# Performance work log

Hardware: AMD Instinct MI355X
Metric: run time of the kernel (lower is better)

Reference implementation:

```python
import jax, jax.numpy as jnp
import numpy as np

D_MODEL = 256
N_HEADS = 4
WINDOW = 8
DECAY = 0.9
STEP_SIZE = 0.5


def _linear(x, w, b):
    # torch nn.Linear: y = x @ w.T + b, w: [out, in]
    return jnp.einsum('...i,oi->...o', x, w) + b


def _layernorm(x, scale, bias, eps=1e-5):
    mu = jnp.mean(x, axis=-1, keepdims=True)
    var = jnp.var(x, axis=-1, keepdims=True)
    return (x - mu) * jax.lax.rsqrt(var + eps) * scale + bias


def _ema(x, decay):
    # ema[t] = decay*ema[t-1] + (1-decay)*x[t], ema[-1]=0
    # (exactly the causal conv with weights (1-d)*d^i from the torch code)
    def step(c, xt):
        c = decay * c + (1.0 - decay) * xt
        return c, c
    _, ys = jax.lax.scan(step, jnp.zeros_like(x[:, 0]), jnp.swapaxes(x, 0, 1))
    return jnp.swapaxes(ys, 0, 1)


def setup_inputs() -> dict:
    key = jax.random.key(0)
    ks = iter(jax.random.split(key, 40))
    B, T, D = 8, 1024, D_MODEL
    s = 0.02
    inp = {
        'parallel_repr': jax.random.normal(next(ks), (B, T, D), jnp.float32),
        'sequential_state': jax.random.normal(next(ks), (B, D), jnp.float32),
        'trajectory_summary': jax.random.normal(next(ks), (B, D), jnp.float32),
        # MultiheadAttention params
        'in_proj_w': jax.random.normal(next(ks), (3 * D, D), jnp.float32) * s,
        'in_proj_b': jnp.zeros((3 * D,), jnp.float32),
        'out_proj_w': jax.random.normal(next(ks), (D, D), jnp.float32) * s,
        'out_proj_b': jnp.zeros((D,), jnp.float32),
        # depthwise causal conv (local history)
        'conv_w': jax.random.normal(next(ks), (D, 1, WINDOW), jnp.float32) * s,
        'conv_b': jnp.zeros((D,), jnp.float32),
        # parallel_to_sequential / sequential_to_parallel
        'p2s_w': jax.random.normal(next(ks), (D, D), jnp.float32) * s,
        'p2s_b': jnp.zeros((D,), jnp.float32),
        's2p_w': jax.random.normal(next(ks), (D, D), jnp.float32) * s,
        's2p_b': jnp.zeros((D,), jnp.float32),
        # transition MLP: 3D -> 2D -> D
        'trans_w1': jax.random.normal(next(ks), (2 * D, 3 * D), jnp.float32) * s,
        'trans_b1': jnp.zeros((2 * D,), jnp.float32),
        'trans_w2': jax.random.normal(next(ks), (D, 2 * D), jnp.float32) * s,
        'trans_b2': jnp.zeros((D,), jnp.float32),
        # FFN: D -> 4D -> D
        'ffn_w1': jax.random.normal(next(ks), (4 * D, D), jnp.float32) * s,
        'ffn_b1': jnp.zeros((4 * D,), jnp.float32),
        'ffn_w2': jax.random.normal(next(ks), (D, 4 * D), jnp.float32) * s,
        'ffn_b2': jnp.zeros((D,), jnp.float32),
        # LayerNorms
        'ln1_s': jnp.ones((D,), jnp.float32), 'ln1_b': jnp.zeros((D,), jnp.float32),
        'ln2_s': jnp.ones((D,), jnp.float32), 'ln2_b': jnp.zeros((D,), jnp.float32),
        'ln3_s': jnp.ones((D,), jnp.float32), 'ln3_b': jnp.zeros((D,), jnp.float32),
        'ln4_s': jnp.ones((D,), jnp.float32), 'ln4_b': jnp.zeros((D,), jnp.float32),
    }
    return inp


def _forward(parallel_repr, sequential_state,
             in_proj_w, in_proj_b, out_proj_w, out_proj_b,
             conv_w, conv_b, p2s_w, p2s_b, s2p_w, s2p_b,
             trans_w1, trans_b1, trans_w2, trans_b2,
             ffn_w1, ffn_b1, ffn_w2, ffn_b2,
             ln1_s, ln1_b, ln2_s, ln2_b, ln3_s, ln3_b, ln4_s, ln4_b):
    B, T, D = parallel_repr.shape
    H, hd = N_HEADS, D // N_HEADS

    # --- causal self-attention (nn.MultiheadAttention, batch_first) ---
    qkv = _linear(parallel_repr, in_proj_w, in_proj_b)
    q, k, v = jnp.split(qkv, 3, axis=-1)
    q = q.reshape(B, T, H, hd)
    k = k.reshape(B, T, H, hd)
    v = v.reshape(B, T, H, hd)
    scores = jnp.einsum('bqhd,bkhd->bhqk', q, k) / jnp.sqrt(jnp.asarray(hd, q.dtype))
    causal = jnp.triu(jnp.ones((T, T), bool), 1)
    scores = jnp.where(causal, jnp.finfo(scores.dtype).min, scores)
    attn = jax.nn.softmax(scores, axis=-1)
    attn_out = jnp.einsum('bhqk,bkhd->bqhd', attn, v).reshape(B, T, D)
    attn_out = _linear(attn_out, out_proj_w, out_proj_b)
    x = _layernorm(parallel_repr + attn_out, ln1_s, ln1_b)

    # --- depthwise causal conv (local history) ---
    xt = jnp.swapaxes(x, 1, 2)  # [B, D, T]
    xt_pad = jnp.pad(xt, ((0, 0), (0, 0), (WINDOW - 1, 0)))
    local = jax.lax.conv_general_dilated(
        xt_pad, conv_w, window_strides=(1,), padding='VALID',
        dimension_numbers=('NCH', 'OIH', 'NCH'), feature_group_count=D)
    local_history = jnp.swapaxes(local + conv_b[None, :, None], 1, 2)  # [B, T, D]

    # --- global EMA summary ---
    global_summary = _ema(x, DECAY)

    # --- transition deltas + cumsum state integration ---
    parallel_guidance = _linear(x, p2s_w, p2s_b)
    combined = jnp.concatenate([x + 0.3 * parallel_guidance, local_history, global_summary], axis=-1)
    h = jax.nn.gelu(_linear(combined, trans_w1, trans_b1), approximate=False)
    deltas = _linear(h, trans_w2, trans_b2)
    states = sequential_state[:, None, :] + jnp.cumsum(deltas, axis=1) * STEP_SIZE
    states = _layernorm(states, ln3_s, ln3_b)

    # --- FFN with sequential guidance ---
    seq_guidance = _linear(states, s2p_w, s2p_b)
    f = jax.nn.gelu(_linear(x + 0.3 * seq_guidance, ffn_w1, ffn_b1), approximate=False)
    ffn_out = _linear(f, ffn_w2, ffn_b2)
    x = _layernorm(x + ffn_out, ln2_s, ln2_b)

    final_sequential_state = _layernorm(states[:, -1, :], ln4_s, ln4_b)
    final_trajectory_summary = global_summary[:, -1, :]
    return x, final_sequential_state, final_trajectory_summary


def reference(parallel_repr, sequential_state, trajectory_summary,
              in_proj_w, in_proj_b, out_proj_w, out_proj_b,
              conv_w, conv_b, p2s_w, p2s_b, s2p_w, s2p_b,
              trans_w1, trans_b1, trans_w2, trans_b2,
              ffn_w1, ffn_b1, ffn_w2, ffn_b2,
              ln1_s, ln1_b, ln2_s, ln2_b, ln3_s, ln3_b, ln4_s, ln4_b):
    # trajectory_summary is accepted by the torch forward but never used.
    return _forward(parallel_repr, sequential_state,
                    in_proj_w, in_proj_b, out_proj_w, out_proj_b,
                    conv_w, conv_b, p2s_w, p2s_b, s2p_w, s2p_b,
                    trans_w1, trans_b1, trans_w2, trans_b2,
                    ffn_w1, ffn_b1, ffn_w2, ffn_b2,
                    ln1_s, ln1_b, ln2_s, ln2_b, ln3_s, ln3_b, ln4_s, ln4_b)
```

## Files before the change

### kernel.cpp

```cpp
#include <hip/hip_runtime.h>
#include <math.h>

typedef unsigned short u16;
typedef __attribute__((ext_vector_type(8))) short bf16x8;
typedef __attribute__((ext_vector_type(4))) float f32x4;

#define D_MODEL 256
#define T_SZ 1024
constexpr size_t S_ELT = (size_t)8192 * 256;
constexpr size_t MB = 1024 * 1024;

constexpr size_t OFF_QK = 0;
constexpr size_t OFF_VT = 8 * MB;
constexpr size_t OFF_ATTN = 12 * MB;
constexpr size_t OFF_X = 16 * MB;
constexpr size_t OFF_XBF = 24 * MB;
constexpr size_t OFF_COMB = 28 * MB;
constexpr size_t OFF_XP = 36 * MB;
constexpr size_t OFF_H = 40 * MB;
constexpr size_t OFF_FB = 48 * MB;
constexpr size_t OFF_STATES = 56 * MB;
constexpr size_t OFF_FFNIN = 60 * MB;
constexpr size_t OFF_F = 64 * MB;
constexpr size_t OFF_PRBF = 80 * MB;
constexpr size_t OFF_WB = 84 * MB;
constexpr size_t OFF_SCR = 88 * MB;

constexpr int WB_INPROJ = 0;
constexpr int WB_OUTPROJ = 196608;
constexpr int WB_P2S = 262144;
constexpr int WB_S2P = 327680;
constexpr int WB_T1 = 393216;
constexpr int WB_T2 = 786432;
constexpr int WB_F1 = 917504;
constexpr int WB_F2 = 1179648;
constexpr int WB_TOTAL = 1441792;
constexpr int PR_TOTAL = 2097152;

__device__ __forceinline__ u16 f2bf(float f) {
  unsigned int u = __float_as_uint(f);
  u += 0x7fff + ((u >> 16) & 1);
  return (u16)(u >> 16);
}
__device__ __forceinline__ float bf2f(u16 s) {
  return __uint_as_float(((unsigned int)s) << 16);
}

__device__ __forceinline__ void glds16(const u16* g, u16* l) {
  __builtin_amdgcn_global_load_lds(
      (const __attribute__((address_space(1))) void*)g,
      (__attribute__((address_space(3))) void*)l, 16, 0, 0);
}

__device__ __forceinline__ float block_reduce_sum(float v, float* tmp) {
#pragma unroll
  for (int o = 32; o > 0; o >>= 1) v += __shfl_down(v, o);
  const int lane = threadIdx.x & 63, wid = threadIdx.x >> 6;
  if (lane == 0) tmp[wid] = v;
  __syncthreads();
  v = tmp[0] + tmp[1] + tmp[2] + tmp[3];
  __syncthreads();
  return v;
}

__global__ __launch_bounds__(256)
void wconv_kernel(const float* w0, const float* w1, const float* w2,
                  const float* w3, const float* w4, const float* w5,
                  const float* w6, const float* w7, const float* pr,
                  u16* __restrict__ wb, u16* __restrict__ prb) {
  const int idx4 = (blockIdx.x * 256 + threadIdx.x) * 4;
  if (idx4 < WB_TOTAL) {
    const int offs[9] = {WB_INPROJ, WB_OUTPROJ, WB_P2S,  WB_S2P, WB_T1,
                         WB_T2,     WB_F1,      WB_F2,   WB_TOTAL};
    const float* srcs[8] = {w0, w1, w2, w3, w4, w5, w6, w7};
    int seg = 0;
    while (idx4 >= offs[seg + 1]) ++seg;
    float4 v = *(const float4*)(srcs[seg] + (idx4 - offs[seg]));
    unsigned int lo = (unsigned int)f2bf(v.x) | ((unsigned int)f2bf(v.y) << 16);
    unsigned int hi = (unsigned int)f2bf(v.z) | ((unsigned int)f2bf(v.w) << 16);
    *(uint2*)(wb + idx4) = make_uint2(lo, hi);
  } else {
    const int i4 = idx4 - WB_TOTAL;
    if (i4 < PR_TOTAL) {
      float4 v = *(const float4*)(pr + i4);
      unsigned int lo = (unsigned int)f2bf(v.x) | ((unsigned int)f2bf(v.y) << 16);
      unsigned int hi = (unsigned int)f2bf(v.z) | ((unsigned int)f2bf(v.w) << 16);
      *(uint2*)(prb + i4) = make_uint2(lo, hi);
    }
  }
}

enum { EPI_NONE = 0, EPI_GELU = 1, EPI_ADDSCALE = 2 };

template <int EPI, int BM, int BN, bool OUTBF, bool VSPLIT>
__global__ __launch_bounds__(256, 4)
void mgemm(const u16* __restrict__ A1, int lda1, const u16* __restrict__ A2,
           int lda2, int ksplit, const u16* __restrict__ W1, int ldw1,
           const u16* __restrict__ W2, int ldw2, int woff2, int K,
           const float* __restrict__ bias, void* __restrict__ Cv, int ldc,
           const float* __restrict__ addsrc, u16* __restrict__ vt) {
  __shared__ u16 As[BM * 64];
  __shared__ u16 Bs[BN * 64];
  const int tid = threadIdx.x;
  const int w = tid >> 6, lane = tid & 63;
  const int ln = lane & 15, quad = lane >> 4;
  const int m0 = blockIdx.x * BM;
  const int n0 = blockIdx.y * BN;
  constexpr int MT = BM / 64;
  constexpr int NT = BN / 16;
  const int wm = w * (MT * 16);
  constexpr int APW = BM / 64;
  constexpr int BPW = BN / 64;

  f32x4 acc[MT][NT] = {};

  const int grow = lane >> 2;
  const int gk8 = (lane & 3) * 8;

  for (int k0 = 0; k0 < K; k0 += 64) {
#pragma unroll
    for (int s = 0; s < 2; ++s) {
      const int kb = k0 + s * 32;
      const bool r1 = kb < ksplit;
      const u16* Ab = r1 ? A1 : A2;
      const int alda = r1 ? lda1 : lda2;
      const int ak = r1 ? kb : kb - ksplit;
#pragma unroll
      for (int p = 0; p < APW; ++p) {
        const int g = w * APW + p;
        glds16(Ab + (size_t)(m0 + g * 16 + grow) * alda + ak + gk8,
               As + s * BM * 32 + g * 512);
      }
      const u16* Wb = r1 ? W1 : W2;
      const int wlda = r1 ? ldw1 : ldw2;
      const int wk = r1 ? kb : kb - woff2;
#pragma unroll
      for (int p = 0; p < BPW; ++p) {
        const int g = w * BPW + p;
        glds16(Wb + (size_t)(n0 + g * 16 + grow) * wlda + wk + gk8,
               Bs + s * BN * 32 + g * 512);
      }
    }
    __syncthreads();
#pragma unroll
    for (int s = 0; s < 2; ++s) {
      const u16* abase = As + s * BM * 32 + (wm >> 4) * 512 + ln * 32 + quad * 8;
      const u16* bbase = Bs + s * BN * 32 + ln * 32 + quad * 8;
      bf16x8 af[MT], bv[NT];
#pragma unroll
      for (int i = 0; i < MT; ++i) af[i] = *(const bf16x8*)(abase + i * 512);
#pragma unroll
      for (int j = 0; j < NT; ++j) bv[j] = *(const bf16x8*)(bbase + j * 512);
#pragma unroll
      for (int i = 0; i < MT; ++i)
#pragma unroll
        for (int j = 0; j < NT; ++j)
          acc[i][j] = __builtin_amdgcn_mfma_f32_16x16x32_bf16(af[i], bv[j],
                                                              acc[i][j], 0, 0, 0);
    }
    __syncthreads();
  }

#pragma unroll
  for (int i = 0; i < MT; ++i)
#pragma unroll
    for (int j = 0; j < NT; ++j) {
      const int col = n0 + j * 16 + ln;
      const float bsv = bias[col];
      const int row0 = m0 + wm + i * 16 + quad * 4;
      float vals[4];
#pragma unroll
      for (int r = 0; r < 4; ++r) {
        float v = acc[i][j][r] + bsv;
        if (EPI == EPI_GELU) v = 0.5f * v * (1.0f + erff(v * 0.70710678f));
        if (EPI == EPI_ADDSCALE)
          v = addsrc[(size_t)(row0 + r) * 256 + col] + 0.3f * v;
        vals[r] = v;
      }
      if (VSPLIT && col >= 512) {
        ushort4 pk;
        pk.x = f2bf(vals[0]); pk.y = f2bf(vals[1]);
        pk.z = f2bf(vals[2]); pk.w = f2bf(vals[3]);
        *(ushort4*)(vt + (size_t)((row0 >> 10) * 256 + (col - 512)) * T_SZ +
                    (row0 & 1023)) = pk;
      } else if (OUTBF) {
#pragma unroll
        for (int r = 0; r < 4; ++r)
          ((u16*)Cv)[(size_t)(row0 + r) * ldc + col] = f2bf(vals[r]);
      } else {
#pragma unroll
        for (int r = 0; r < 4; ++r)
          ((float*)Cv)[(size_t)(row0 + r) * ldc + col] = vals[r];
      }
    }
}

__global__ __launch_bounds__(256)
void attn_flash(const u16* __restrict__ qk, const u16* __restrict__ vt,
                u16* __restrict__ outp) {
  __shared__ u16 Ps[4][16][72];
  const int tid = threadIdx.x;
  const int w = tid >> 6, lane = tid & 63;
  const int ln = lane & 15, quad = lane >> 4, kq8 = quad * 8;
  const int wu = blockIdx.x * 4 + w;
  const int bh = wu >> 6, s = wu & 63;
  const int qt = (s & 1) ? (63 - (s >> 1)) : (s >> 1);
  const int q0 = qt * 16;
  const int b = bh >> 2, h = bh & 3;
  const u16* base = qk + (size_t)b * T_SZ * 512;
  const u16* vbase = vt + (size_t)bh * 64 * T_SZ;

  bf16x8 qf[2];
#pragma unroll
  for (int ks = 0; ks < 2; ++ks)
    qf[ks] = *(const bf16x8*)(base + (size_t)(q0 + ln) * 512 + h * 64 +
                              ks * 32 + kq8);
  const short ob = (short)0x3F80;
  const bf16x8 ones = {ob, ob, ob, ob, ob, ob, ob, ob};

  f32x4 O[4] = {};
  f32x4 l_acc = {};
  const int ntiles = (qt >> 2) + 1;
  for (int jt = 0; jt < ntiles; ++jt) {
    const int c0 = jt * 64;
    f32x4 sv[4] = {};
#pragma unroll
    for (int ks = 0; ks < 2; ++ks)
#pragma unroll
      for (int j = 0; j < 4; ++j) {
        bf16x8 kf = *(const bf16x8*)(base + (size_t)(c0 + j * 16 + ln) * 512 +
                                     256 + h * 64 + ks * 32 + kq8);
        sv[j] = __builtin_amdgcn_mfma_f32_16x16x32_bf16(qf[ks], kf, sv[j], 0, 0, 0);
      }
    const bool need_mask = (c0 + 63 > q0);
#pragma unroll
    for (int j = 0; j < 4; ++j)
#pragma unroll
      for (int r = 0; r < 4; ++r) {
        float p = __expf(sv[j][r] * 0.125f);
        if (need_mask && (c0 + j * 16 + ln > q0 + quad * 4 + r)) p = 0.f;
        Ps[w][quad * 4 + r][j * 16 + ln] = f2bf(p);
      }
#pragma unroll
    for (int ks = 0; ks < 2; ++ks) {
      bf16x8 pf = *(const bf16x8*)&Ps[w][ln][ks * 32 + kq8];
      l_acc = __builtin_amdgcn_mfma_f32_16x16x32_bf16(pf, ones, l_acc, 0, 0, 0);
#pragma unroll
      for (int j = 0; j < 4; ++j) {
        bf16x8 vf = *(const bf16x8*)(vbase + (size_t)(j * 16 + ln) * T_SZ +
                                     c0 + ks * 32 + kq8);
        O[j] = __builtin_amdgcn_mfma_f32_16x16x32_bf16(pf, vf, O[j], 0, 0, 0);
      }
    }
  }
  u16* op = outp + (size_t)b * T_SZ * 256;
#pragma unroll
  for (int r = 0; r < 4; ++r) {
    const float inv = 1.f / l_acc[r];
#pragma unroll
    for (int j = 0; j < 4; ++j)
      op[(size_t)(q0 + quad * 4 + r) * 256 + h * 64 + j * 16 + ln] =
          f2bf(O[j][r] * inv);
  }
}

__device__ __forceinline__ float ln_finish(float v, float s1, float s2,
                                           float g, float bb) {
  float mean = s1 * (1.f / 256.f);
  float var = s2 * (1.f / 256.f) - mean * mean;
  return (v - mean) * rsqrtf(var + 1e-5f) * g + bb;
}

__global__ __launch_bounds__(256)
void ln_add_kernel(const float* __restrict__ a, const float* __restrict__ addsrc,
                   const float* __restrict__ g, const float* __restrict__ bb,
                   float* __restrict__ outp, u16* __restrict__ obf) {
  __shared__ float tmp[4];
  const size_t row = blockIdx.x;
  const int d = threadIdx.x;
  float v = a[row * 256 + d] + addsrc[row * 256 + d];
  float s1 = block_reduce_sum(v, tmp);
  float s2 = block_reduce_sum(v * v, tmp);
  float y = ln_finish(v, s1, s2, g[d], bb[d]);
  outp[row * 256 + d] = y;
  if (obf) obf[row * 256 + d] = f2bf(y);
}

__global__ __launch_bounds__(256)
void ln34_kernel(const float* __restrict__ deltas, const float* __restrict__ scr,
                 const float* __restrict__ seq, const float* __restrict__ g3,
                 const float* __restrict__ b3, const float* __restrict__ g4,
                 const float* __restrict__ b4, u16* __restrict__ st,
                 float* __restrict__ fss) {
  __shared__ float tmp[4];
  const int row = blockIdx.x;
  const int b = row >> 10, t = row & 1023;
  const int d = threadIdx.x;
  float v = seq[b * 256 + d] +
            0.5f * (deltas[(size_t)row * 256 + d] +
                    scr[(size_t)(b * 32 + (t >> 5)) * 256 + d]);
  float s1 = block_reduce_sum(v, tmp);
  float s2 = block_reduce_sum(v * v, tmp);
  float y = ln_finish(v, s1, s2, g3[d], b3[d]);
  st[(size_t)row * 256 + d] = f2bf(y);
  if (t == 1023) {
    float t1s = block_reduce_sum(y, tmp);
    float t2s = block_reduce_sum(y * y, tmp);
    fss[b * 256 + d] = ln_finish(y, t1s, t2s, g4[d], b4[d]);
  }
}

__global__ __launch_bounds__(256)
void emaconv_kernel(const float* __restrict__ x, const float* __restrict__ cw,
                    const float* __restrict__ cb, u16* __restrict__ comb,
                    float* __restrict__ scr) {
  const int bc = blockIdx.x;
  const int b = bc >> 5, ch = bc & 31;
  const int d = threadIdx.x;
  const int t0 = ch * 32;
  float wreg[8];
#pragma unroll
  for (int j = 0; j < 8; ++j) wreg[j] = cw[d * 8 + j];
  const float bias = cb[d];
  float xw[8];
#pragma unroll
  for (int j = 0; j < 7; ++j) {
    const int ts = t0 - 7 + j;
    xw[j] = (ts >= 0) ? x[(size_t)(b * T_SZ + ts) * 256 + d] : 0.f;
  }
  float c = 0.f;
#pragma unroll
  for (int tl = 0; tl < 32; ++tl) {
    const size_t row = (size_t)(b * T_SZ + t0 + tl);
    xw[7] = x[row * 256 + d];
    float conv = bias;
#pragma unroll
    for (int j = 0; j < 8; ++j) conv = fmaf(xw[j], wreg[j], conv);
    c = 0.9f * c + 0.1f * xw[7];
    comb[row * 512 + d] = f2bf(conv);
    comb[row * 512 + 256 + d] = f2bf(c);
#pragma unroll
    for (int j = 0; j < 7; ++j) xw[j] = xw[j + 1];
  }
  scr[(size_t)bc * 256 + d] = c;
}

__global__ __launch_bounds__(256)
void ema_b_kernel(float* __restrict__ scr) {
  const int b = blockIdx.x, d = threadIdx.x;
  const float q32 = 0.03433683820292512f;
  float carry = 0.f;
  for (int ch = 0; ch < 32; ++ch) {
    const size_t idx = (size_t)(b * 32 + ch) * 256 + d;
    float e = scr[idx];
    scr[idx] = carry;
    carry = e + q32 * carry;
  }
}

__global__ __launch_bounds__(256)
void ema_c_kernel(u16* __restrict__ comb, const float* __restrict__ scr,
                  float* __restrict__ fts) {
  const int row = blockIdx.x;
  const int b = row >> 10, t = row & 1023;
  const int d = threadIdx.x;
  const int ch = t >> 5, tl = t & 31;
  float carry = scr[(size_t)(b * 32 + ch) * 256 + d];
  float l = bf2f(comb[(size_t)row * 512 + 256 + d]);
  float y = fmaf(__powf(0.9f, (float)(tl + 1)), carry, l);
  comb[(size_t)row * 512 + 256 + d] = f2bf(y);
  if (t == 1023) fts[b * 256 + d] = y;
}

__global__ __launch_bounds__(256)
void cs_a_kernel(float* __restrict__ deltas, float* __restrict__ scr) {
  const int bc = blockIdx.x;
  const int b = bc >> 5, ch = bc & 31;
  const int d = threadIdx.x;
  const int t0 = ch * 32;
  float c = 0.f;
  for (int tl = 0; tl < 32; ++tl) {
    const size_t idx = (size_t)(b * T_SZ + t0 + tl) * 256 + d;
    c += deltas[idx];
    deltas[idx] = c;
  }
  scr[(size_t)bc * 256 + d] = c;
}

__global__ __launch_bounds__(256)
void cs_b_kernel(float* __restrict__ scr) {
  const int b = blockIdx.x, d = threadIdx.x;
  float carry = 0.f;
  for (int ch = 0; ch < 32; ++ch) {
    const size_t idx = (size_t)(b * 32 + ch) * 256 + d;
    float e = scr[idx];
    scr[idx] = carry;
    carry += e;
  }
}

extern "C" void kernel_launch(void* const* d_in, const int* in_sizes, int n_in,
                              void* d_out, int out_size, void* d_ws,
                              size_t ws_size, hipStream_t stream) {
  (void)in_sizes; (void)n_in; (void)out_size; (void)ws_size;
  const float* parallel_repr = (const float*)d_in[0];
  const float* sequential_state = (const float*)d_in[1];
  const float* in_proj_b = (const float*)d_in[4];
  const float* out_proj_b = (const float*)d_in[6];
  const float* conv_w = (const float*)d_in[7];
  const float* conv_b = (const float*)d_in[8];
  const float* p2s_b = (const float*)d_in[10];
  const float* s2p_b = (const float*)d_in[12];
  const float* trans_b1 = (const float*)d_in[14];
  const float* trans_b2 = (const float*)d_in[16];
  const float* ffn_b1 = (const float*)d_in[18];
  const float* ffn_b2 = (const float*)d_in[20];
  const float* ln1_s = (const float*)d_in[21];
  const float* ln1_b = (const float*)d_in[22];
  const float* ln2_s = (const float*)d_in[23];
  const float* ln2_b = (const float*)d_in[24];
  const float* ln3_s = (const float*)d_in[25];
  const float* ln3_b = (const float*)d_in[26];
  const float* ln4_s = (const float*)d_in[27];
  const float* ln4_b = (const float*)d_in[28];

  char* ws = (char*)d_ws;
  u16* qk_bf = (u16*)(ws + OFF_QK);
  u16* vt = (u16*)(ws + OFF_VT);
  u16* attn_bf = (u16*)(ws + OFF_ATTN);
  float* x = (float*)(ws + OFF_X);
  u16* x_bf = (u16*)(ws + OFF_XBF);
  u16* comb = (u16*)(ws + OFF_COMB);
  u16* xp_bf = (u16*)(ws + OFF_XP);
  u16* h_bf = (u16*)(ws + OFF_H);
  float* fbuf = (float*)(ws + OFF_FB);
  u16* states_bf = (u16*)(ws + OFF_STATES);
  u16* ffn_in = (u16*)(ws + OFF_FFNIN);
  u16* f_bf = (u16*)(ws + OFF_F);
  u16* pr_bf = (u16*)(ws + OFF_PRBF);
  u16* wb = (u16*)(ws + OFF_WB);
  float* scr = (float*)(ws + OFF_SCR);
  float* out = (float*)d_out;
  float* out_fss = out + S_ELT;
  float* out_fts = out + S_ELT + 2048;

  const dim3 blk(256);

  wconv_kernel<<<3456, blk, 0, stream>>>(
      (const float*)d_in[3], (const float*)d_in[5], (const float*)d_in[9],
      (const float*)d_in[11], (const float*)d_in[13], (const float*)d_in[15],
      (const float*)d_in[17], (const float*)d_in[19], parallel_repr, wb, pr_bf);
  mgemm<EPI_NONE, 128, 64, true, true><<<dim3(64, 12), blk, 0, stream>>>(
      pr_bf, 256, pr_bf, 256, 256, wb + WB_INPROJ, 256, wb + WB_INPROJ, 256, 0,
      256, in_proj_b, qk_bf, 512, nullptr, vt);
  attn_flash<<<512, blk, 0, stream>>>(qk_bf, vt, attn_bf);
  mgemm<EPI_NONE, 64, 64, false, false><<<dim3(128, 4), blk, 0, stream>>>(
      attn_bf, 256, attn_bf, 256, 256, wb + WB_OUTPROJ, 256, wb + WB_OUTPROJ,
      256, 0, 256, out_proj_b, fbuf, 256, nullptr, nullptr);
  ln_add_kernel<<<8192, blk, 0, stream>>>(parallel_repr, fbuf, ln1_s, ln1_b, x,
                                          x_bf);
  emaconv_kernel<<<256, blk, 0, stream>>>(x, conv_w, conv_b, comb, scr);
  ema_b_kernel<<<8, blk, 0, stream>>>(scr);
  ema_c_kernel<<<8192, blk, 0, stream>>>(comb, scr, out_fts);
  mgemm<EPI_ADDSCALE, 64, 64, true, false><<<dim3(128, 4), blk, 0, stream>>>(
      x_bf, 256, x_bf, 256, 256, wb + WB_P2S, 256, wb + WB_P2S, 256, 0, 256,
      p2s_b, xp_bf, 256, x, nullptr);
  mgemm<EPI_GELU, 128, 64, true, false><<<dim3(64, 8), blk, 0, stream>>>(
      xp_bf, 256, comb, 512, 256, wb + WB_T1, 768, wb + WB_T1, 768, 0, 768,
      trans_b1, h_bf, 512, nullptr, nullptr);
  mgemm<EPI_NONE, 64, 64, false, false><<<dim3(128, 4), blk, 0, stream>>>(
      h_bf, 512, h_bf, 512, 512, wb + WB_T2, 512, wb + WB_T2, 512, 0, 512,
      trans_b2, fbuf, 256, nullptr, nullptr);
  cs_a_kernel<<<256, blk, 0, stream>>>(fbuf, scr);
  cs_b_kernel<<<8, blk, 0, stream>>>(scr);
  ln34_kernel<<<8192, blk, 0, stream>>>(fbuf, scr, sequential_state, ln3_s,
                                        ln3_b, ln4_s, ln4_b, states_bf, out_fss);
  mgemm<EPI_ADDSCALE, 64, 64, true, false><<<dim3(128, 4), blk, 0, stream>>>(
      states_bf, 256, states_bf, 256, 256, wb + WB_S2P, 256, wb + WB_S2P, 256,
      0, 256, s2p_b, ffn_in, 256, x, nullptr);
  mgemm<EPI_GELU, 128, 64, true, false><<<dim3(64, 16), blk, 0, stream>>>(
      ffn_in, 256, ffn_in, 256, 256, wb + WB_F1, 256, wb + WB_F1, 256, 0, 256,
      ffn_b1, f_bf, 1024, nullptr, nullptr);
  mgemm<EPI_NONE, 64, 64, false, false><<<dim3(128, 4), blk, 0, stream>>>(
      f_bf, 1024, f_bf, 1024, 1024, wb + WB_F2, 1024, wb + WB_F2, 1024, 0,
      1024, ffn_b2, fbuf, 256, nullptr, nullptr);
  ln_add_kernel<<<8192, blk, 0, stream>>>(x, fbuf, ln2_s, ln2_b, out, nullptr);
}
```

Baseline: 283.3 us.

## Fold p2s/s2p linear layers into downstream GEMM weights and drop scan kernels

The p2s and s2p projections feed only linear layers (trans_w1 and ffn_w1), so their weights are pre-multiplied into combined weight matrices by a small MFMA kernel (wfold_mfma). This removes two full activation GEMMs and their intermediate buffers. The FFN1 GEMM now takes a K=512 concatenation of x and states. The two 8-block serial carry-scan kernels are also removed: each row recomputes its carry by looping over prior chunk sums inside ema_c and ln34. The cost is extra weight-prep work, a larger K in FFN1, redundant carry loops per row, and some extra rounding error from the folded bf16 weights.

```diff
diff --git a/kernel.cpp b/kernel.cpp
--- a/kernel.cpp
+++ b/kernel.cpp
@@ -16,15 +16,19 @@
 constexpr size_t OFF_X = 16 * MB;
 constexpr size_t OFF_XBF = 24 * MB;
 constexpr size_t OFF_COMB = 28 * MB;
-constexpr size_t OFF_XP = 36 * MB;
-constexpr size_t OFF_H = 40 * MB;
-constexpr size_t OFF_FB = 48 * MB;
-constexpr size_t OFF_STATES = 56 * MB;
-constexpr size_t OFF_FFNIN = 60 * MB;
-constexpr size_t OFF_F = 64 * MB;
-constexpr size_t OFF_PRBF = 80 * MB;
-constexpr size_t OFF_WB = 84 * MB;
-constexpr size_t OFF_SCR = 88 * MB;
+constexpr size_t OFF_H = 36 * MB;
+constexpr size_t OFF_FB = 44 * MB;
+constexpr size_t OFF_STATES = 52 * MB;
+constexpr size_t OFF_F = 56 * MB;
+constexpr size_t OFF_PRBF = 72 * MB;
+constexpr size_t OFF_WB = 76 * MB;
+constexpr size_t OFF_P2ST = 79 * MB;
+constexpr size_t OFF_S2PT = 79 * MB + 163840;
+constexpr size_t OFF_W1X = 80 * MB;
+constexpr size_t OFF_W1S = 80 * MB + 262144;
+constexpr size_t OFF_B1X = 81 * MB;
+constexpr size_t OFF_B1S = 81 * MB + 4096;
+constexpr size_t OFF_SCR = 82 * MB;
 
 constexpr int WB_INPROJ = 0;
 constexpr int WB_OUTPROJ = 196608;
@@ -36,6 +40,7 @@
 constexpr int WB_F2 = 1179648;
 constexpr int WB_TOTAL = 1441792;
 constexpr int PR_TOTAL = 2097152;
+constexpr int TR_TOTAL = 163840;
 
 __device__ __forceinline__ u16 f2bf(float f) {
   unsigned int u = __float_as_uint(f);
@@ -67,7 +72,9 @@
 void wconv_kernel(const float* w0, const float* w1, const float* w2,
                   const float* w3, const float* w4, const float* w5,
                   const float* w6, const float* w7, const float* pr,
-                  u16* __restrict__ wb, u16* __restrict__ prb) {
+                  const float* p2sb, const float* s2pb, u16* __restrict__ wb,
+                  u16* __restrict__ prb, u16* __restrict__ p2sT,
+                  u16* __restrict__ s2pT) {
   const int idx4 = (blockIdx.x * 256 + threadIdx.x) * 4;
   if (idx4 < WB_TOTAL) {
     const int offs[9] = {WB_INPROJ, WB_OUTPROJ, WB_P2S,  WB_S2P, WB_T1,
@@ -79,18 +86,99 @@
     unsigned int lo = (unsigned int)f2bf(v.x) | ((unsigned int)f2bf(v.y) << 16);
     unsigned int hi = (unsigned int)f2bf(v.z) | ((unsigned int)f2bf(v.w) << 16);
     *(uint2*)(wb + idx4) = make_uint2(lo, hi);
+  } else if (idx4 < WB_TOTAL + PR_TOTAL) {
+    const int i4 = idx4 - WB_TOTAL;
+    float4 v = *(const float4*)(pr + i4);
+    unsigned int lo = (unsigned int)f2bf(v.x) | ((unsigned int)f2bf(v.y) << 16);
+    unsigned int hi = (unsigned int)f2bf(v.z) | ((unsigned int)f2bf(v.w) << 16);
+    *(uint2*)(prb + i4) = make_uint2(lo, hi);
   } else {
-    const int i4 = idx4 - WB_TOTAL;
-    if (i4 < PR_TOTAL) {
-      float4 v = *(const float4*)(pr + i4);
-      unsigned int lo = (unsigned int)f2bf(v.x) | ((unsigned int)f2bf(v.y) << 16);
-      unsigned int hi = (unsigned int)f2bf(v.z) | ((unsigned int)f2bf(v.w) << 16);
-      *(uint2*)(prb + i4) = make_uint2(lo, hi);
-    }
-  }
-}
-
-enum { EPI_NONE = 0, EPI_GELU = 1, EPI_ADDSCALE = 2 };
+    int e = idx4 - (WB_TOTAL + PR_TOTAL);
+    if (e >= TR_TOTAL) return;
+    const bool second = e >= (TR_TOTAL / 2);
+    if (second) e -= TR_TOTAL / 2;
+    const float* src = second ? w3 : w2;
+    const float* bias = second ? s2pb : p2sb;
+    u16* dst = second ? s2pT : p2sT;
+    const int j = e >> 8, k0 = e & 255;
+    u16 h[4];
+#pragma unroll
+    for (int q = 0; q < 4; ++q) {
+      const int k = k0 + q;
+      float v = 0.f;
+      if (j < 256) v = src[k * 256 + j];
+      else if (j == 256) v = bias[k];
+      h[q] = f2bf(v);
+    }
+    unsigned int lo = (unsigned int)h[0] | ((unsigned int)h[1] << 16);
+    unsigned int hi = (unsigned int)h[2] | ((unsigned int)h[3] << 16);
+    *(uint2*)(dst + e) = make_uint2(lo, hi);
+  }
+}
+
+__global__ __launch_bounds__(256, 4)
+void wfold_mfma(const u16* __restrict__ wb, const u16* __restrict__ p2sT,
+                const u16* __restrict__ s2pT, const float* __restrict__ tb1,
+                const float* __restrict__ fb1, u16* __restrict__ w1x,
+                u16* __restrict__ w1s, float* __restrict__ b1x,
+                float* __restrict__ b1s) {
+  __shared__ u16 As[64 * 64];
+  __shared__ u16 Bs[64 * 64];
+  const int tid = threadIdx.x;
+  const int w = tid >> 6, lane = tid & 63;
+  const int ln = lane & 15, quad = lane >> 4;
+  const bool m1 = blockIdx.x >= 8;
+  const int m0 = (m1 ? (blockIdx.x - 8) : blockIdx.x) * 64;
+  const int n0 = blockIdx.y * 64;
+  const u16* A = m1 ? (wb + WB_F1) : (wb + WB_T1);
+  const int lda = m1 ? 256 : 768;
+  const u16* B = m1 ? s2pT : p2sT;
+  const float* tb = m1 ? fb1 : tb1;
+  u16* wout = m1 ? w1s : w1x;
+  float* bout = m1 ? b1s : b1x;
+  const int wm = w * 16;
+  f32x4 acc[4] = {};
+  const int grow = lane >> 2, gk8 = (lane & 3) * 8;
+
+  for (int k0 = 0; k0 < 256; k0 += 64) {
+#pragma unroll
+    for (int s = 0; s < 2; ++s) {
+      glds16(A + (size_t)(m0 + w * 16 + grow) * lda + k0 + s * 32 + gk8,
+             As + s * 2048 + w * 512);
+      glds16(B + (size_t)(n0 + w * 16 + grow) * 256 + k0 + s * 32 + gk8,
+             Bs + s * 2048 + w * 512);
+    }
+    __syncthreads();
+#pragma unroll
+    for (int s = 0; s < 2; ++s) {
+      bf16x8 af = *(const bf16x8*)(As + s * 2048 + w * 512 + ln * 32 + quad * 8);
+#pragma unroll
+      for (int j = 0; j < 4; ++j) {
+        bf16x8 bv = *(const bf16x8*)(Bs + s * 2048 + j * 512 + ln * 32 + quad * 8);
+        acc[j] = __builtin_amdgcn_mfma_f32_16x16x32_bf16(af, bv, acc[j], 0, 0, 0);
+      }
+    }
+    __syncthreads();
+  }
+#pragma unroll
+  for (int j = 0; j < 4; ++j) {
+    const int col = n0 + j * 16 + ln;
+    const int row0 = m0 + wm + quad * 4;
+    if (col < 256) {
+#pragma unroll
+      for (int r = 0; r < 4; ++r) {
+        float add = m1 ? 0.f : bf2f(wb[WB_T1 + (size_t)(row0 + r) * 768 + col]);
+        wout[(size_t)(row0 + r) * 256 + col] = f2bf(add + 0.3f * acc[j][r]);
+      }
+    } else if (col == 256) {
+#pragma unroll
+      for (int r = 0; r < 4; ++r)
+        bout[row0 + r] = tb[row0 + r] + 0.3f * acc[j][r];
+    }
+  }
+}
+
+enum { EPI_NONE = 0, EPI_GELU = 1 };
 
 template <int EPI, int BM, int BN, bool OUTBF, bool VSPLIT>
 __global__ __launch_bounds__(256, 4)
@@ -98,7 +186,7 @@
            int lda2, int ksplit, const u16* __restrict__ W1, int ldw1,
            const u16* __restrict__ W2, int ldw2, int woff2, int K,
            const float* __restrict__ bias, void* __restrict__ Cv, int ldc,
-           const float* __restrict__ addsrc, u16* __restrict__ vt) {
+           u16* __restrict__ vt) {
   __shared__ u16 As[BM * 64];
   __shared__ u16 Bs[BN * 64];
   const int tid = threadIdx.x;
@@ -173,8 +261,6 @@
       for (int r = 0; r < 4; ++r) {
         float v = acc[i][j][r] + bsv;
         if (EPI == EPI_GELU) v = 0.5f * v * (1.0f + erff(v * 0.70710678f));
-        if (EPI == EPI_ADDSCALE)
-          v = addsrc[(size_t)(row0 + r) * 256 + col] + 0.3f * v;
         vals[r] = v;
       }
       if (VSPLIT && col >= 512) {
@@ -296,9 +382,12 @@
   const int row = blockIdx.x;
   const int b = row >> 10, t = row & 1023;
   const int d = threadIdx.x;
+  const int ch = t >> 5;
+  float carry = 0.f;
+  for (int j = 0; j < ch; ++j)
+    carry += scr[(size_t)(b * 32 + j) * 256 + d];
   float v = seq[b * 256 + d] +
-            0.5f * (deltas[(size_t)row * 256 + d] +
-                    scr[(size_t)(b * 32 + (t >> 5)) * 256 + d]);
+            0.5f * (deltas[(size_t)row * 256 + d] + carry);
   float s1 = block_reduce_sum(v, tmp);
   float s2 = block_reduce_sum(v * v, tmp);
   float y = ln_finish(v, s1, s2, g3[d], b3[d]);
@@ -346,26 +435,16 @@
 }
 
 __global__ __launch_bounds__(256)
-void ema_b_kernel(float* __restrict__ scr) {
-  const int b = blockIdx.x, d = threadIdx.x;
-  const float q32 = 0.03433683820292512f;
-  float carry = 0.f;
-  for (int ch = 0; ch < 32; ++ch) {
-    const size_t idx = (size_t)(b * 32 + ch) * 256 + d;
-    float e = scr[idx];
-    scr[idx] = carry;
-    carry = e + q32 * carry;
-  }
-}
-
-__global__ __launch_bounds__(256)
 void ema_c_kernel(u16* __restrict__ comb, const float* __restrict__ scr,
                   float* __restrict__ fts) {
   const int row = blockIdx.x;
   const int b = row >> 10, t = row & 1023;
   const int d = threadIdx.x;
   const int ch = t >> 5, tl = t & 31;
-  float carry = scr[(size_t)(b * 32 + ch) * 256 + d];
+  const float q32 = 0.03433683820292512f;
+  float carry = 0.f;
+  for (int j = 0; j < ch; ++j)
+    carry = q32 * carry + scr[(size_t)(b * 32 + j) * 256 + d];
   float l = bf2f(comb[(size_t)row * 512 + 256 + d]);
   float y = fmaf(__powf(0.9f, (float)(tl + 1)), carry, l);
   comb[(size_t)row * 512 + 256 + d] = f2bf(y);
@@ -385,18 +464,6 @@
     deltas[idx] = c;
   }
   scr[(size_t)bc * 256 + d] = c;
-}
-
-__global__ __launch_bounds__(256)
-void cs_b_kernel(float* __restrict__ scr) {
-  const int b = blockIdx.x, d = threadIdx.x;
-  float carry = 0.f;
-  for (int ch = 0; ch < 32; ++ch) {
-    const size_t idx = (size_t)(b * 32 + ch) * 256 + d;
-    float e = scr[idx];
-    scr[idx] = carry;
-    carry += e;
-  }
 }
 
 extern "C" void kernel_launch(void* const* d_in, const int* in_sizes, int n_in,
@@ -431,14 +498,18 @@
   float* x = (float*)(ws + OFF_X);
   u16* x_bf = (u16*)(ws + OFF_XBF);
   u16* comb = (u16*)(ws + OFF_COMB);
-  u16* xp_bf = (u16*)(ws + OFF_XP);
   u16* h_bf = (u16*)(ws + OFF_H);
   float* fbuf = (float*)(ws + OFF_FB);
   u16* states_bf = (u16*)(ws + OFF_STATES);
-  u16* ffn_in = (u16*)(ws + OFF_FFNIN);
   u16* f_bf = (u16*)(ws + OFF_F);
   u16* pr_bf = (u16*)(ws + OFF_PRBF);
   u16* wb = (u16*)(ws + OFF_WB);
+  u16* p2sT = (u16*)(ws + OFF_P2ST);
+  u16* s2pT = (u16*)(ws + OFF_S2PT);
+  u16* w1x = (u16*)(ws + OFF_W1X);
+  u16* w1s = (u16*)(ws + OFF_W1S);
+  float* b1x = (float*)(ws + OFF_B1X);
+  float* b1s = (float*)(ws + OFF_B1S);
   float* scr = (float*)(ws + OFF_SCR);
   float* out = (float*)d_out;
   float* out_fss = out + S_ELT;
@@ -446,43 +517,38 @@
 
   const dim3 blk(256);
 
-  wconv_kernel<<<3456, blk, 0, stream>>>(
+  wconv_kernel<<<3617, blk, 0, stream>>>(
       (const float*)d_in[3], (const float*)d_in[5], (const float*)d_in[9],
       (const float*)d_in[11], (const float*)d_in[13], (const float*)d_in[15],
-      (const float*)d_in[17], (const float*)d_in[19], parallel_repr, wb, pr_bf);
+      (const float*)d_in[17], (const float*)d_in[19], parallel_repr, p2s_b,
+      s2p_b, wb, pr_bf, p2sT, s2pT);
+  wfold_mfma<<<dim3(24, 5), blk, 0, stream>>>(wb, p2sT, s2pT, trans_b1, ffn_b1,
+                                              w1x, w1s, b1x, b1s);
   mgemm<EPI_NONE, 128, 64, true, true><<<dim3(64, 12), blk, 0, stream>>>(
       pr_bf, 256, pr_bf, 256, 256, wb + WB_INPROJ, 256, wb + WB_INPROJ, 256, 0,
-      256, in_proj_b, qk_bf, 512, nullptr, vt);
+      256, in_proj_b, qk_bf, 512, vt);
   attn_flash<<<512, blk, 0, stream>>>(qk_bf, vt, attn_bf);
   mgemm<EPI_NONE, 64, 64, false, false><<<dim3(128, 4), blk, 0, stream>>>(
       attn_bf, 256, attn_bf, 256, 256, wb + WB_OUTPROJ, 256, wb + WB_OUTPROJ,
-      256, 0, 256, out_proj_b, fbuf, 256, nullptr, nullptr);
+      256, 0, 256, out_proj_b, fbuf, 256, nullptr);
   ln_add_kernel<<<8192, blk, 0, stream>>>(parallel_repr, fbuf, ln1_s, ln1_b, x,
                                           x_bf);
   emaconv_kernel<<<256, blk, 0, stream>>>(x, conv_w, conv_b, comb, scr);
-  ema_b_kernel<<<8, blk, 0, stream>>>(scr);
   ema_c_kernel<<<8192, blk, 0, stream>>>(comb, scr, out_fts);
-  mgemm<EPI_ADDSCALE, 64, 64, true, false><<<dim3(128, 4), blk, 0, stream>>>(
-      x_bf, 256, x_bf, 256, 256, wb + WB_P2S, 256, wb + WB_P2S, 256, 0, 256,
-      p2s_b, xp_bf, 256, x, nullptr);
   mgemm<EPI_GELU, 128, 64, true, false><<<dim3(64, 8), blk, 0, stream>>>(
-      xp_bf, 256, comb, 512, 256, wb + WB_T1, 768, wb + WB_T1, 768, 0, 768,
-      trans_b1, h_bf, 512, nullptr, nullptr);
+      x_bf, 256, comb, 512, 256, w1x, 256, wb + WB_T1, 768, 0, 768, b1x, h_bf,
+      512, nullptr);
   mgemm<EPI_NONE, 64, 64, false, false><<<dim3(128, 4), blk, 0, stream>>>(
       h_bf, 512, h_bf, 512, 512, wb + WB_T2, 512, wb + WB_T2, 512, 0, 512,
-      trans_b2, fbuf, 256, nullptr, nullptr);
+      trans_b2, fbuf, 256, nullptr);
   cs_a_kernel<<<256, blk, 0, stream>>>(fbuf, scr);
-  cs_b_kernel<<<8, blk, 0, stream>>>(scr);
   ln34_kernel<<<8192, blk, 0, stream>>>(fbuf, scr, sequential_state, ln3_s,
                                         ln3_b, ln4_s, ln4_b, states_bf, out_fss);
-  mgemm<EPI_ADDSCALE, 64, 64, true, false><<<dim3(128, 4), blk, 0, stream>>>(
-      states_bf, 256, states_bf, 256, 256, wb + WB_S2P, 256, wb + WB_S2P, 256,
-      0, 256, s2p_b, ffn_in, 256, x, nullptr);
   mgemm<EPI_GELU, 128, 64, true, false><<<dim3(64, 16), blk, 0, stream>>>(
-      ffn_in, 256, ffn_in, 256, 256, wb + WB_F1, 256, wb + WB_F1, 256, 0, 256,
-      ffn_b1, f_bf, 1024, nullptr, nullptr);
+      x_bf, 256, states_bf, 256, 256, wb + WB_F1, 256, w1s, 256, 256, 512, b1s,
+      f_bf, 1024, nullptr);
   mgemm<EPI_NONE, 64, 64, false, false><<<dim3(128, 4), blk, 0, stream>>>(
       f_bf, 1024, f_bf, 1024, 1024, wb + WB_F2, 1024, wb + WB_F2, 1024, 0,
-      1024, ffn_b2, fbuf, 256, nullptr, nullptr);
+      1024, ffn_b2, fbuf, 256, nullptr);
   ln_add_kernel<<<8192, blk, 0, stream>>>(x, fbuf, ln2_s, ln2_b, out, nullptr);
 }
```

Measured after the change: 312.9 us. 1.1x slower.
